# Kernel optimization log

Hardware: AMD Instinct MI355X
Metric: run time of the kernel (lower is better)

Reference implementation:

```python
import jax, jax.numpy as jnp
import numpy as np

NEG_INF = -1e9  # module uses -1e9 negativeInfinity constant
BS, DA, SL, H = 16, 512, 1024, 8


def setup_inputs() -> dict:
    key = jax.random.key(0)
    ks = jax.random.split(key, 8)
    return {
        "q":    jax.random.normal(ks[0], (BS, DA, SL), dtype=jnp.float32),
        "k_in": jax.random.normal(ks[1], (BS, DA, SL), dtype=jnp.float32),
        "v_in": jax.random.normal(ks[2], (BS, DA, SL), dtype=jnp.float32),
        "k_w":  jax.random.normal(ks[3], (DA, DA), dtype=jnp.float32) * 0.05,
        "k_b":  jax.random.normal(ks[4], (DA,), dtype=jnp.float32) * 0.05,
        "v_w":  jax.random.normal(ks[5], (DA, DA), dtype=jnp.float32) * 0.05,
        "v_b":  jax.random.normal(ks[6], (DA,), dtype=jnp.float32) * 0.05,
        "gbn_gamma": jnp.ones((H,), dtype=jnp.float32),
        "gbn_bias":  jnp.zeros((H,), dtype=jnp.float32),
        "gbn_m":     jnp.zeros((H,), dtype=jnp.float32),
        "gbn_s":     jnp.ones((H,), dtype=jnp.float32),
        "mask": jax.random.randint(ks[7], (BS, 1, 1, SL), 0, 2, dtype=jnp.int32),
    }


def reference(q, k_in, v_in, k_w, k_b, v_w, v_b, gbn_gamma, gbn_bias, gbn_m, gbn_s, mask):
    bs, da, qsl = q.shape
    h = gbn_gamma.shape[0]
    dh = da // h
    sl = k_in.shape[2]
    mask_b = mask.astype(bool)                 # [bs,1,1,sl] True = masked

    # 1x1 conv1d projections == per-position matmul over channels
    k = jnp.einsum('ok,bks->bos', k_w, k_in) + k_b[None, :, None]   # [bs,da,sl]
    v = jnp.einsum('ov,bvs->bos', v_w, v_in) + v_b[None, :, None]   # [bs,dva,sl]
    dva = v.shape[1]
    dvh = dva // h

    qh = q.reshape(bs, h, dh, qsl).transpose(0, 1, 3, 2)   # [bs,h,qsl,dh]
    kh = k.reshape(bs, h, dh, sl)                          # [bs,h,dh,sl]
    vh = v.reshape(bs, h, dvh, sl).transpose(0, 1, 3, 2)   # [bs,h,sl,dvh]

    scores = jnp.einsum('bhqd,bhds->bhqs', qh, kh)         # [bs,h,qsl,sl]

    # GhostBatchNorm1d(features=h) in eval mode: per-head affine normalization
    scores = (scores - gbn_m[None, :, None, None]) / gbn_s[None, :, None, None]
    scores = scores * gbn_gamma[None, :, None, None] + gbn_bias[None, :, None, None]

    mask_k = mask_b                           # [bs,1,1,sl]  mask key positions (selfAttention fill)
    mask_q = jnp.swapaxes(mask_b, 2, 3)       # [bs,1,sl,1]  mask query rows (transposed fill)
    scores = jnp.where(mask_k, NEG_INF, scores)
    scores = jnp.where(mask_q, NEG_INF, scores)

    w = jax.nn.softmax(scores, axis=-1)
    w = jnp.where(mask_q, 0.0, w)             # v_weights.masked_fill(mask, 0)

    out = jnp.einsum('bhqs,bhsd->bhqd', w, vh)             # [bs,h,qsl,dvh]
    out = out.transpose(0, 1, 3, 2).reshape(bs, dva, qsl)  # back to channels-first
    return out
```

## Files before the change

### kernel.cpp

```cpp
#include <hip/hip_runtime.h>

typedef _Float16 f16;
typedef _Float16 h8_t __attribute__((ext_vector_type(8)));
typedef _Float16 h4_t __attribute__((ext_vector_type(4)));
typedef float f32x4 __attribute__((ext_vector_type(4)));
typedef float f32x16 __attribute__((ext_vector_type(16)));

#define BS 16
#define DA 512
#define SL 1024
#define NH 8
#define DH 64

template <int MODE>
__global__ __launch_bounds__(256) void fused_proj(const float* __restrict__ Wg,
                                                  const float* __restrict__ Xin,
                                                  const float* __restrict__ bias,
                                                  f16* __restrict__ outg) {
  constexpr int MT = MODE ? SL : DA;
  constexpr int NT = MODE ? DA : SL;
  __shared__ f16 Wl[128 * 40];
  __shared__ f16 Xl[128 * 40];
  __shared__ float Xf32[32 * 132];
  const int b = blockIdx.z;
  const int m0 = blockIdx.x * 128;
  const int n0 = blockIdx.y * 128;
  const int o_base = MODE ? n0 : m0;
  const int s_base = MODE ? m0 : n0;
  const int t = threadIdx.x;
  const int w = t >> 6, lane = t & 63, lr = lane & 15, lq = lane >> 4;
  const int wm = (w >> 1) * 64, wn = (w & 1) * 64;

  f32x4 acc[4][4] = {};

  for (int kt = 0; kt < 16; ++kt) {
    const int c0 = kt * 32;
    __syncthreads();
#pragma unroll
    for (int p = 0; p < 4; ++p) {
      const int idx = p * 256 + t;
      const int row = idx >> 3, cq = (idx & 7) * 4;
      const float4 v = *(const float4*)&Wg[(size_t)(o_base + row) * DA + c0 + cq];
      h4_t hv;
      hv[0] = (f16)v.x; hv[1] = (f16)v.y; hv[2] = (f16)v.z; hv[3] = (f16)v.w;
      *(h4_t*)&Wl[row * 40 + cq] = hv;
    }
#pragma unroll
    for (int p = 0; p < 4; ++p) {
      const int idx = p * 256 + t;
      const int cc = idx >> 5, s4 = (idx & 31) * 4;
      const float4 v = *(const float4*)&Xin[((size_t)b * DA + c0 + cc) * SL + s_base + s4];
      *(float4*)&Xf32[cc * 132 + s4] = v;
    }
    __syncthreads();
    {
      const int srow = t >> 1, cb = (t & 1) * 16;
      h8_t lo, hi;
#pragma unroll
      for (int u = 0; u < 8; ++u) lo[u] = (f16)Xf32[(cb + u) * 132 + srow];
#pragma unroll
      for (int u = 0; u < 8; ++u) hi[u] = (f16)Xf32[(cb + 8 + u) * 132 + srow];
      *(h8_t*)&Xl[srow * 40 + cb] = lo;
      *(h8_t*)&Xl[srow * 40 + cb + 8] = hi;
    }
    __syncthreads();
    const f16* Al = MODE ? Xl : Wl;
    const f16* Bl = MODE ? Wl : Xl;
    h8_t af[4], bf[4];
#pragma unroll
    for (int i = 0; i < 4; ++i) af[i] = *(const h8_t*)&Al[(wm + i * 16 + lr) * 40 + lq * 8];
#pragma unroll
    for (int j = 0; j < 4; ++j) bf[j] = *(const h8_t*)&Bl[(wn + j * 16 + lr) * 40 + lq * 8];
#pragma unroll
    for (int i = 0; i < 4; ++i)
#pragma unroll
      for (int j = 0; j < 4; ++j)
        acc[i][j] = __builtin_amdgcn_mfma_f32_16x16x32_f16(af[i], bf[j], acc[i][j], 0, 0, 0);
  }

#pragma unroll
  for (int i = 0; i < 4; ++i) {
    const int gmb = m0 + wm + i * 16 + lq * 4;
    float bm[4] = {0.f, 0.f, 0.f, 0.f};
    if (MODE == 0) {
      const float4 b4 = *(const float4*)&bias[gmb];
      bm[0] = b4.x; bm[1] = b4.y; bm[2] = b4.z; bm[3] = b4.w;
    }
#pragma unroll
    for (int j = 0; j < 4; ++j) {
      const int gn = n0 + wn + j * 16 + lr;
      const float bn = (MODE == 1) ? bias[gn] : 0.f;
      h4_t hv;
#pragma unroll
      for (int r = 0; r < 4; ++r) {
        const float val = acc[i][j][r] + (MODE == 0 ? bm[r] : bn);
        hv[r] = (f16)val;
      }
      *(h4_t*)&outg[((size_t)b * NT + gn) * MT + gmb] = hv;
    }
  }
}

__global__ __launch_bounds__(256, 2) void attn_kernel(
    const float* __restrict__ qg, const f16* __restrict__ kp, const f16* __restrict__ vp,
    const float* __restrict__ gamma, const float* __restrict__ gbns,
    const int* __restrict__ maskg, float* __restrict__ outg) {
  __shared__ __align__(16) char smem[36864];
  f16* KV = (f16*)smem;
  float* Osh = (float*)smem;

  const int bh = blockIdx.x, b = bh >> 3, h = bh & 7;
  const int i0 = blockIdx.y * 256;
  const int t = threadIdx.x, w = t >> 6, lane = t & 63;
  const int l5 = lane & 31, hf = lane >> 5;
  const float scale = gamma[h] / gbns[h] * 1.44269504088896f;

  h8_t qf[2][4];
#pragma unroll
  for (int im = 0; im < 2; ++im)
#pragma unroll
    for (int ks = 0; ks < 4; ++ks) {
      h8_t v;
#pragma unroll
      for (int u = 0; u < 8; ++u) {
        const int d = ks * 16 + hf * 8 + u;
        v[u] = (f16)(qg[((size_t)b * DA + h * DH + d) * SL + i0 + w * 64 + im * 32 + l5] * scale);
      }
      qf[im][ks] = v;
    }

  const int srow = t >> 3;
  const int c8 = (t & 7) * 8;

  uint4 rk[2], rv[2];
#pragma unroll
  for (int p = 0; p < 2; ++p) {
    const int row = p * 32 + srow;
    rk[p] = *(const uint4*)&kp[((size_t)b * SL + row) * DA + h * DH + c8];
    rv[p] = *(const uint4*)&vp[((size_t)b * DA + h * DH + row) * SL + c8];
  }
  {
    f16* K0 = KV;
    f16* V0 = KV + 4608;
#pragma unroll
    for (int p = 0; p < 2; ++p) {
      const int row = p * 32 + srow;
      const int rowp = (row & ~12) | ((row & 4) << 1) | ((row & 8) >> 1);
      *(uint4*)&K0[rowp * 72 + c8] = rk[p];
      *(uint4*)&V0[row * 72 + c8] = rv[p];
    }
  }
  __syncthreads();

  float m_i[2] = {-3e38f, -3e38f}, l_i[2] = {0.f, 0.f};
  f32x16 acc[2][2] = {};

  for (int jt = 0; jt < 16; ++jt) {
    const int j0 = jt * 64;
    const f16* Kc = KV + (jt & 1) * 9216;
    const f16* Vc = Kc + 4608;

    if (jt < 15) {
      const int jn = j0 + 64;
#pragma unroll
      for (int p = 0; p < 2; ++p) {
        const int row = p * 32 + srow;
        rk[p] = *(const uint4*)&kp[((size_t)b * SL + jn + row) * DA + h * DH + c8];
        rv[p] = *(const uint4*)&vp[((size_t)b * DA + h * DH + row) * SL + jn + c8];
      }
    }
    int4 mq[2][4];
#pragma unroll
    for (int mj = 0; mj < 2; ++mj)
#pragma unroll
      for (int q = 0; q < 4; ++q)
        mq[mj][q] = *(const int4*)&maskg[b * SL + j0 + mj * 32 + (q >> 1) * 16 + hf * 8 + (q & 1) * 4];

    f32x16 sa[2][2] = {};
#pragma unroll
    for (int ks = 0; ks < 4; ++ks)
#pragma unroll
      for (int mj = 0; mj < 2; ++mj) {
        const h8_t kf = *(const h8_t*)&Kc[(mj * 32 + l5) * 72 + ks * 16 + hf * 8];
#pragma unroll
        for (int im = 0; im < 2; ++im)
          sa[im][mj] = __builtin_amdgcn_mfma_f32_32x32x16_f16(kf, qf[im][ks], sa[im][mj], 0, 0, 0);
      }

#pragma unroll
    for (int mj = 0; mj < 2; ++mj)
#pragma unroll
      for (int q = 0; q < 4; ++q) {
        const int4 m4 = mq[mj][q];
#pragma unroll
        for (int im = 0; im < 2; ++im) {
          if (m4.x) sa[im][mj][q * 4 + 0] = -1e9f;
          if (m4.y) sa[im][mj][q * 4 + 1] = -1e9f;
          if (m4.z) sa[im][mj][q * 4 + 2] = -1e9f;
          if (m4.w) sa[im][mj][q * 4 + 3] = -1e9f;
        }
      }

    float alpha[2];
#pragma unroll
    for (int im = 0; im < 2; ++im) {
      float mx = sa[im][0][0];
#pragma unroll
      for (int e = 1; e < 16; ++e) mx = fmaxf(mx, sa[im][0][e]);
#pragma unroll
      for (int e = 0; e < 16; ++e) mx = fmaxf(mx, sa[im][1][e]);
      mx = fmaxf(mx, __shfl_xor(mx, 32));
      const float mn = fmaxf(m_i[im], mx);
      alpha[im] = __builtin_amdgcn_exp2f(m_i[im] - mn);
      m_i[im] = mn;
      float rs = 0.f;
#pragma unroll
      for (int mj = 0; mj < 2; ++mj)
#pragma unroll
        for (int e = 0; e < 16; ++e) {
          const float pv = __builtin_amdgcn_exp2f(sa[im][mj][e] - mn);
          sa[im][mj][e] = pv;
          rs += pv;
        }
      rs += __shfl_xor(rs, 32);
      l_i[im] = l_i[im] * alpha[im] + rs;
#pragma unroll
      for (int nd = 0; nd < 2; ++nd)
#pragma unroll
        for (int e = 0; e < 16; ++e) acc[im][nd][e] *= alpha[im];
    }

#pragma unroll
    for (int jk = 0; jk < 4; ++jk) {
      const int mj = jk >> 1, g = jk & 1;
      h8_t pf[2];
#pragma unroll
      for (int im = 0; im < 2; ++im) {
        h8_t pk;
#pragma unroll
        for (int u = 0; u < 8; ++u) pk[u] = (f16)sa[im][mj][g * 8 + u];
        pf[im] = pk;
      }
#pragma unroll
      for (int nd = 0; nd < 2; ++nd) {
        const h8_t vf = *(const h8_t*)&Vc[(nd * 32 + l5) * 72 + jk * 16 + hf * 8];
#pragma unroll
        for (int im = 0; im < 2; ++im)
          acc[im][nd] = __builtin_amdgcn_mfma_f32_32x32x16_f16(vf, pf[im], acc[im][nd], 0, 0, 0);
      }
    }

    if (jt < 15) {
      f16* Kn = KV + ((jt + 1) & 1) * 9216;
      f16* Vn = Kn + 4608;
#pragma unroll
      for (int p = 0; p < 2; ++p) {
        const int row = p * 32 + srow;
        const int rowp = (row & ~12) | ((row & 4) << 1) | ((row & 8) >> 1);
        *(uint4*)&Kn[rowp * 72 + c8] = rk[p];
        *(uint4*)&Vn[row * 72 + c8] = rv[p];
      }
      __syncthreads();
    }
  }

  float fac[2];
#pragma unroll
  for (int im = 0; im < 2; ++im) {
    const int mo = maskg[b * SL + i0 + w * 64 + im * 32 + l5];
    fac[im] = mo ? 0.f : 1.f / l_i[im];
  }
  __syncthreads();

#pragma unroll
  for (int nd = 0; nd < 2; ++nd) {
#pragma unroll
    for (int im = 0; im < 2; ++im)
#pragma unroll
      for (int e = 0; e < 16; ++e) {
        const int dl = (e & 3) + 8 * (e >> 2) + 4 * hf;
        Osh[dl * 256 + w * 64 + im * 32 + l5] = acc[im][nd][e] * fac[im];
      }
    __syncthreads();
#pragma unroll
    for (int pass = 0; pass < 8; ++pass) {
      const int row = pass * 4 + w;
      const int i4 = lane * 4;
      const float4 o = *(const float4*)&Osh[row * 256 + i4];
      *(float4*)&outg[((size_t)b * DA + h * DH + nd * 32 + row) * SL + i0 + i4] = o;
    }
    __syncthreads();
  }
}

extern "C" void kernel_launch(void* const* d_in, const int* in_sizes, int n_in,
                              void* d_out, int out_size, void* d_ws, size_t ws_size,
                              hipStream_t stream) {
  const float* q     = (const float*)d_in[0];
  const float* k_in  = (const float*)d_in[1];
  const float* v_in  = (const float*)d_in[2];
  const float* k_w   = (const float*)d_in[3];
  const float* k_b   = (const float*)d_in[4];
  const float* v_w   = (const float*)d_in[5];
  const float* v_b   = (const float*)d_in[6];
  const float* gamma = (const float*)d_in[7];
  const float* gbns  = (const float*)d_in[10];
  const int*   mask  = (const int*)d_in[11];
  float* out = (float*)d_out;

  const size_t NEL = (size_t)BS * SL * DA;
  f16* kpw = (f16*)d_ws;
  f16* vpw = kpw + NEL;

  fused_proj<0><<<dim3(4, 8, BS), 256, 0, stream>>>(k_w, k_in, k_b, kpw);
  fused_proj<1><<<dim3(8, 4, BS), 256, 0, stream>>>(v_w, v_in, v_b, vpw);
  attn_kernel<<<dim3(BS * NH, SL / 256), 256, 0, stream>>>(q, kpw, vpw, gamma, gbns, mask, out);
}
```

Before: 260.2 us.

## Software-pipeline QK^T ahead of softmax-PV and merge K/V projection launches

The attention loop is unrolled by two with ping-pong score registers, so the QK^T MFMAs for the next tile are issued before the softmax and PV of the current tile, overlapping matrix work with exp/reduction work. The two projection kernels are merged into one launch with a runtime mode bit and a higher occupancy hint, removing one kernel launch and letting K and V blocks share the GPU. The costs are more live registers from the second score buffer, extra barriers per tile, and runtime branching in the projection kernel that used to be resolved at compile time.

```diff
diff --git a/kernel.cpp b/kernel.cpp
--- a/kernel.cpp
+++ b/kernel.cpp
@@ -12,21 +12,27 @@
 #define NH 8
 #define DH 64
 
-template <int MODE>
-__global__ __launch_bounds__(256) void fused_proj(const float* __restrict__ Wg,
-                                                  const float* __restrict__ Xin,
-                                                  const float* __restrict__ bias,
-                                                  f16* __restrict__ outg) {
-  constexpr int MT = MODE ? SL : DA;
-  constexpr int NT = MODE ? DA : SL;
+__global__ __launch_bounds__(256, 4) void fused_proj_both(
+    const float* __restrict__ k_w, const float* __restrict__ v_w,
+    const float* __restrict__ k_in, const float* __restrict__ v_in,
+    const float* __restrict__ k_b, const float* __restrict__ v_b,
+    f16* __restrict__ kp, f16* __restrict__ vp) {
   __shared__ f16 Wl[128 * 40];
   __shared__ f16 Xl[128 * 40];
   __shared__ float Xf32[32 * 132];
-  const int b = blockIdx.z;
-  const int m0 = blockIdx.x * 128;
-  const int n0 = blockIdx.y * 128;
-  const int o_base = MODE ? n0 : m0;
-  const int s_base = MODE ? m0 : n0;
+  const int mode = blockIdx.z & 1;
+  const int b = blockIdx.z >> 1;
+  const int x = blockIdx.x;
+  const int m0 = (mode ? (x >> 2) : (x & 3)) * 128;
+  const int n0 = (mode ? (x & 3) : (x >> 2)) * 128;
+  const float* Wg = mode ? v_w : k_w;
+  const float* Xin = mode ? v_in : k_in;
+  const float* bias = mode ? v_b : k_b;
+  f16* outg = mode ? vp : kp;
+  const int MT = mode ? SL : DA;
+  const int NT = mode ? DA : SL;
+  const int o_base = mode ? n0 : m0;
+  const int s_base = mode ? m0 : n0;
   const int t = threadIdx.x;
   const int w = t >> 6, lane = t & 63, lr = lane & 15, lq = lane >> 4;
   const int wm = (w >> 1) * 64, wn = (w & 1) * 64;
@@ -64,8 +70,8 @@
       *(h8_t*)&Xl[srow * 40 + cb + 8] = hi;
     }
     __syncthreads();
-    const f16* Al = MODE ? Xl : Wl;
-    const f16* Bl = MODE ? Wl : Xl;
+    const f16* Al = mode ? Xl : Wl;
+    const f16* Bl = mode ? Wl : Xl;
     h8_t af[4], bf[4];
 #pragma unroll
     for (int i = 0; i < 4; ++i) af[i] = *(const h8_t*)&Al[(wm + i * 16 + lr) * 40 + lq * 8];
@@ -82,18 +88,18 @@
   for (int i = 0; i < 4; ++i) {
     const int gmb = m0 + wm + i * 16 + lq * 4;
     float bm[4] = {0.f, 0.f, 0.f, 0.f};
-    if (MODE == 0) {
+    if (mode == 0) {
       const float4 b4 = *(const float4*)&bias[gmb];
       bm[0] = b4.x; bm[1] = b4.y; bm[2] = b4.z; bm[3] = b4.w;
     }
 #pragma unroll
     for (int j = 0; j < 4; ++j) {
       const int gn = n0 + wn + j * 16 + lr;
-      const float bn = (MODE == 1) ? bias[gn] : 0.f;
+      const float bn = mode ? bias[gn] : 0.f;
       h4_t hv;
 #pragma unroll
       for (int r = 0; r < 4; ++r) {
-        const float val = acc[i][j][r] + (MODE == 0 ? bm[r] : bn);
+        const float val = acc[i][j][r] + (mode ? bn : bm[r]);
         hv[r] = (f16)val;
       }
       *(h4_t*)&outg[((size_t)b * NT + gn) * MT + gmb] = hv;
@@ -115,7 +121,11 @@
   const int l5 = lane & 31, hf = lane >> 5;
   const float scale = gamma[h] / gbns[h] * 1.44269504088896f;
 
+  float m_i[2] = {-3e38f, -3e38f}, l_i[2] = {0.f, 0.f};
+  f32x16 acc[2][2] = {};
+  uint4 rk[2], rv[2];
   h8_t qf[2][4];
+
 #pragma unroll
   for (int im = 0; im < 2; ++im)
 #pragma unroll
@@ -131,52 +141,30 @@
 
   const int srow = t >> 3;
   const int c8 = (t & 7) * 8;
-
-  uint4 rk[2], rv[2];
-#pragma unroll
-  for (int p = 0; p < 2; ++p) {
-    const int row = p * 32 + srow;
-    rk[p] = *(const uint4*)&kp[((size_t)b * SL + row) * DA + h * DH + c8];
-    rv[p] = *(const uint4*)&vp[((size_t)b * DA + h * DH + row) * SL + c8];
-  }
-  {
-    f16* K0 = KV;
-    f16* V0 = KV + 4608;
-#pragma unroll
-    for (int p = 0; p < 2; ++p) {
-      const int row = p * 32 + srow;
-      const int rowp = (row & ~12) | ((row & 4) << 1) | ((row & 8) >> 1);
-      *(uint4*)&K0[rowp * 72 + c8] = rk[p];
-      *(uint4*)&V0[row * 72 + c8] = rv[p];
-    }
-  }
-  __syncthreads();
-
-  float m_i[2] = {-3e38f, -3e38f}, l_i[2] = {0.f, 0.f};
-  f32x16 acc[2][2] = {};
-
-  for (int jt = 0; jt < 16; ++jt) {
-    const int j0 = jt * 64;
-    const f16* Kc = KV + (jt & 1) * 9216;
-    const f16* Vc = Kc + 4608;
-
-    if (jt < 15) {
-      const int jn = j0 + 64;
-#pragma unroll
-      for (int p = 0; p < 2; ++p) {
-        const int row = p * 32 + srow;
-        rk[p] = *(const uint4*)&kp[((size_t)b * SL + jn + row) * DA + h * DH + c8];
-        rv[p] = *(const uint4*)&vp[((size_t)b * DA + h * DH + row) * SL + jn + c8];
-      }
-    }
-    int4 mq[2][4];
-#pragma unroll
-    for (int mj = 0; mj < 2; ++mj)
-#pragma unroll
-      for (int q = 0; q < 4; ++q)
-        mq[mj][q] = *(const int4*)&maskg[b * SL + j0 + mj * 32 + (q >> 1) * 16 + hf * 8 + (q & 1) * 4];
-
-    f32x16 sa[2][2] = {};
+  const int row0 = srow, row1 = 32 + srow;
+  const int rowp0 = (row0 & ~12) | ((row0 & 4) << 1) | ((row0 & 8) >> 1);
+  const int rowp1 = (row1 & ~12) | ((row1 & 4) << 1) | ((row1 & 8) >> 1);
+
+  auto gload = [&](int jn) {
+    rk[0] = *(const uint4*)&kp[((size_t)b * SL + jn + row0) * DA + h * DH + c8];
+    rv[0] = *(const uint4*)&vp[((size_t)b * DA + h * DH + row0) * SL + jn + c8];
+    rk[1] = *(const uint4*)&kp[((size_t)b * SL + jn + row1) * DA + h * DH + c8];
+    rv[1] = *(const uint4*)&vp[((size_t)b * DA + h * DH + row1) * SL + jn + c8];
+  };
+  auto swrite = [&](int bi) {
+    f16* Kn = KV + bi * 9216;
+    f16* Vn = Kn + 4608;
+    *(uint4*)&Kn[rowp0 * 72 + c8] = rk[0];
+    *(uint4*)&Vn[row0 * 72 + c8] = rv[0];
+    *(uint4*)&Kn[rowp1 * 72 + c8] = rk[1];
+    *(uint4*)&Vn[row1 * 72 + c8] = rv[1];
+  };
+  auto computeS = [&](f32x16 (&sa)[2][2], int bi) {
+    const f16* Kc = KV + bi * 9216;
+#pragma unroll
+    for (int im = 0; im < 2; ++im)
+#pragma unroll
+      for (int mj = 0; mj < 2; ++mj) sa[im][mj] = (f32x16)(0.f);
 #pragma unroll
     for (int ks = 0; ks < 4; ++ks)
 #pragma unroll
@@ -186,7 +174,17 @@
         for (int im = 0; im < 2; ++im)
           sa[im][mj] = __builtin_amdgcn_mfma_f32_32x32x16_f16(kf, qf[im][ks], sa[im][mj], 0, 0, 0);
       }
-
+  };
+  auto softmax_pv = [&](f32x16 (&sa)[2][2], int jt, int bi) {
+    const int j0 = jt * 64;
+    const f16* Vc = KV + bi * 9216 + 4608;
+    int4 mq[2][4];
+#pragma unroll
+    for (int mj = 0; mj < 2; ++mj)
+#pragma unroll
+      for (int q = 0; q < 4; ++q)
+        mq[mj][q] =
+            *(const int4*)&maskg[b * SL + j0 + mj * 32 + (q >> 1) * 16 + hf * 8 + (q & 1) * 4];
 #pragma unroll
     for (int mj = 0; mj < 2; ++mj)
 #pragma unroll
@@ -200,7 +198,6 @@
           if (m4.w) sa[im][mj][q * 4 + 3] = -1e9f;
         }
       }
-
     float alpha[2];
 #pragma unroll
     for (int im = 0; im < 2; ++im) {
@@ -229,7 +226,6 @@
 #pragma unroll
         for (int e = 0; e < 16; ++e) acc[im][nd][e] *= alpha[im];
     }
-
 #pragma unroll
     for (int jk = 0; jk < 4; ++jk) {
       const int mj = jk >> 1, g = jk & 1;
@@ -249,19 +245,29 @@
           acc[im][nd] = __builtin_amdgcn_mfma_f32_32x32x16_f16(vf, pf[im], acc[im][nd], 0, 0, 0);
       }
     }
-
-    if (jt < 15) {
-      f16* Kn = KV + ((jt + 1) & 1) * 9216;
-      f16* Vn = Kn + 4608;
-#pragma unroll
-      for (int p = 0; p < 2; ++p) {
-        const int row = p * 32 + srow;
-        const int rowp = (row & ~12) | ((row & 4) << 1) | ((row & 8) >> 1);
-        *(uint4*)&Kn[rowp * 72 + c8] = rk[p];
-        *(uint4*)&Vn[row * 72 + c8] = rv[p];
-      }
-      __syncthreads();
-    }
+  };
+
+  gload(0);
+  swrite(0);
+  gload(64);
+  __syncthreads();
+  f32x16 saA[2][2], saB[2][2];
+  computeS(saA, 0);
+
+  for (int tt = 0; tt < 8; ++tt) {
+    const int ta = 2 * tt, tb = 2 * tt + 1;
+    __syncthreads();
+    swrite(1);
+    __syncthreads();
+    computeS(saB, 1);
+    if (ta < 14) gload((ta + 2) * 64);
+    softmax_pv(saA, ta, 0);
+    __syncthreads();
+    if (tb < 15) swrite(0);
+    __syncthreads();
+    if (tb < 15) computeS(saA, 0);
+    if (tb < 14) gload((tb + 2) * 64);
+    softmax_pv(saB, tb, 1);
   }
 
   float fac[2];
@@ -312,7 +318,7 @@
   f16* kpw = (f16*)d_ws;
   f16* vpw = kpw + NEL;
 
-  fused_proj<0><<<dim3(4, 8, BS), 256, 0, stream>>>(k_w, k_in, k_b, kpw);
-  fused_proj<1><<<dim3(8, 4, BS), 256, 0, stream>>>(v_w, v_in, v_b, vpw);
+  fused_proj_both<<<dim3(32, 1, BS * 2), 256, 0, stream>>>(k_w, v_w, k_in, v_in, k_b, v_b,
+                                                           kpw, vpw);
   attn_kernel<<<dim3(BS * NH, SL / 256), 256, 0, stream>>>(q, kpw, vpw, gamma, gbns, mask, out);
 }
```

Result: slower. 331.9 us (+27.5%).
